# Kernel optimization log

Hardware: AMD Instinct MI355X
Metric: run time of the kernel (lower is better)

## Reference

```python
import jax, jax.numpy as jnp
import numpy as np

B, T, D, P = 32, 2048, 256, 100000
MAX_SPAN = 16


def setup_inputs() -> dict:
    key = jax.random.key(0)
    k0, k1, k2, k3, k4, k5 = jax.random.split(key, 6)
    token_embs = jax.random.normal(k0, (B, T, D), dtype=jnp.float32)
    p1_span = jax.random.randint(k1, (P,), 1, MAX_SPAN + 1, dtype=jnp.int32)
    p2_span = jax.random.randint(k2, (P,), 1, MAX_SPAN + 1, dtype=jnp.int32)
    p1_start = jax.random.randint(k3, (P,), 0, T - MAX_SPAN, dtype=jnp.int32)
    p2_start = jax.random.randint(k4, (P,), 0, T - MAX_SPAN, dtype=jnp.int32)
    pair_batch = jax.random.randint(k5, (P,), 0, B, dtype=jnp.int32)
    return {
        "token_embs": token_embs,
        "p1_start": p1_start,
        "p1_span": p1_span,
        "p2_start": p2_start,
        "p2_span": p2_span,
        "pair_batch": pair_batch,
    }


def reference(token_embs, p1_start, p1_span, p2_start, p2_span, pair_batch):
    # token_embs: [B, T, D]; per-pair ranges [start, start+span) within batch row pair_batch.
    # Range mean via exclusive prefix sums: mean = (csum[end] - csum[start]) / span.
    b, t, d = token_embs.shape
    csum = jnp.concatenate(
        [jnp.zeros((b, 1, d), token_embs.dtype), jnp.cumsum(token_embs, axis=1)],
        axis=1,
    )  # [B, T+1, D]

    def span_mean(start, span):
        end = start + span
        s = csum[pair_batch, end] - csum[pair_batch, start]  # [P, D]
        return s / span[:, None].astype(token_embs.dtype)

    p1 = span_mean(p1_start, p1_span)
    p2 = span_mean(p2_start, p2_span)
    return jnp.concatenate([p1, p2], axis=-1)  # [P, 2D]
```

## Files before the change

### kernel.cpp

```cpp
#include <hip/hip_runtime.h>


#define PB_B 32
#define PB_T 2048
#define PB_D 256
#define PB_P 100000
#define NSPAN (2 * PB_P)
#define NWIN 128
#define NBIN (PB_B * NWIN)
#define WROWS 31

typedef float vfloat4 __attribute__((ext_vector_type(4)));

__global__ __launch_bounds__(256) void hist_kernel(
    const int* __restrict__ p1_start, const int* __restrict__ p2_start,
    const int* __restrict__ pair_batch, int* __restrict__ counts)
{
    const int i = blockIdx.x * 256 + threadIdx.x;
    if (i >= PB_P) return;
    const int b = pair_batch[i];
    atomicAdd(&counts[(b << 7) + (p1_start[i] >> 4)], 1);
    atomicAdd(&counts[(b << 7) + (p2_start[i] >> 4)], 1);
}

__global__ __launch_bounds__(256) void scan_bins_kernel(
    const int* __restrict__ counts, int* __restrict__ bin_base,
    int* __restrict__ cursors)
{
    __shared__ int wsum[4];
    const int t = threadIdx.x;
    int local[16];
    int run = 0;
    #pragma unroll
    for (int i = 0; i < 16; ++i) { local[i] = counts[t * 16 + i]; run += local[i]; }

    const int lane = t & 63, wv = t >> 6;
    int incl = run;
    #pragma unroll
    for (int off = 1; off < 64; off <<= 1) {
        int v = __shfl_up(incl, off);
        if (lane >= off) incl += v;
    }
    if (lane == 63) wsum[wv] = incl;
    __syncthreads();
    int base = incl - run;
    for (int i = 0; i < wv; ++i) base += wsum[i];

    int c = base;
    #pragma unroll
    for (int i = 0; i < 16; ++i) {
        bin_base[t * 16 + i] = c;
        cursors[t * 16 + i] = c;
        c += local[i];
    }
    if (t == 255) bin_base[NBIN] = c;
}

__global__ __launch_bounds__(256) void scatter_kernel(
    const int* __restrict__ p1_start, const int* __restrict__ p1_span,
    const int* __restrict__ p2_start, const int* __restrict__ p2_span,
    const int* __restrict__ pair_batch,
    int* __restrict__ cursors, int2* __restrict__ meta)
{
    const int i = blockIdx.x * 256 + threadIdx.x;
    if (i >= PB_P) return;
    const int b = pair_batch[i];
    {
        const int s = p1_start[i];
        const int pos = atomicAdd(&cursors[(b << 7) + (s >> 4)], 1);
        meta[pos] = make_int2(2 * i, (b << 11) + s + (p1_span[i] << 16));
    }
    {
        const int s = p2_start[i];
        const int pos = atomicAdd(&cursors[(b << 7) + (s >> 4)], 1);
        meta[pos] = make_int2(2 * i + 1, (b << 11) + s + (p2_span[i] << 16));
    }
}

__global__ __launch_bounds__(512) void gather_kernel(
    const float* __restrict__ emb, const int2* __restrict__ meta,
    const int* __restrict__ bin_base, float* __restrict__ out)
{
    __shared__ float cs[32 * PB_D];

    const int blk  = (blockIdx.x & 7) * (NBIN / 8) + (blockIdx.x >> 3);
    const int b    = blk >> 7;
    const int row0 = (blk & 127) << 4;

    const float4* __restrict__ g =
        (const float4*)(emb + (((long long)b << 11) + row0) * PB_D);
    float4* l4 = (float4*)cs;
    const int nf4 = WROWS * (PB_D / 4);
    const int nvalid = (PB_T - row0 < WROWS ? PB_T - row0 : WROWS) * (PB_D / 4);
    #pragma unroll
    for (int k = 0; k < 4; ++k) {
        const int i = k * 512 + threadIdx.x;
        if (i < nf4) {
            float4 v = make_float4(0.f, 0.f, 0.f, 0.f);
            if (i < nvalid) v = g[i];
            l4[i] = v;
        }
    }
    __syncthreads();

    if (threadIdx.x < PB_D) {
        const int d = threadIdx.x;
        float run = 0.f;
        #pragma unroll
        for (int r = 0; r < WROWS; ++r) {
            const float v = cs[r * PB_D + d];
            cs[r * PB_D + d] = run;
            run += v;
        }
        cs[WROWS * PB_D + d] = run;
    }
    __syncthreads();

    const int s0 = bin_base[blk], s1 = bin_base[blk + 1];
    const int lane = threadIdx.x & 63, wv = threadIdx.x >> 6;
    for (int s = s0 + wv; s < s1; s += 8) {
        const int2 m = meta[s];
        const int lr = (m.y & 2047) - row0;
        const int n  = m.y >> 16;
        const float4 a = ((const float4*)cs)[lr * (PB_D / 4) + lane];
        const float4 e = ((const float4*)cs)[(lr + n) * (PB_D / 4) + lane];
        const float inv = 1.f / (float)n;
        vfloat4 o = { (e.x - a.x) * inv, (e.y - a.y) * inv,
                      (e.z - a.z) * inv, (e.w - a.w) * inv };
        __builtin_nontemporal_store(o, (vfloat4*)out + (long long)m.x * 64 + lane);
    }
}

extern "C" void kernel_launch(void* const* d_in, const int* in_sizes, int n_in,
                              void* d_out, int out_size, void* d_ws, size_t ws_size,
                              hipStream_t stream) {
    const float* token_embs = (const float*)d_in[0];
    const int* p1_start = (const int*)d_in[1];
    const int* p1_span  = (const int*)d_in[2];
    const int* p2_start = (const int*)d_in[3];
    const int* p2_span  = (const int*)d_in[4];
    const int* pair_batch = (const int*)d_in[5];
    float* out = (float*)d_out;

    int2* meta   = (int2*)d_ws;
    int* counts  = (int*)(meta + NSPAN);
    int* cursors = counts + NBIN;
    int* bin_base = cursors + NBIN;

    (void)hipMemsetAsync(counts, 0, NBIN * sizeof(int), stream);
    const int hb = (PB_P + 255) / 256;
    hist_kernel<<<hb, 256, 0, stream>>>(p1_start, p2_start, pair_batch, counts);
    scan_bins_kernel<<<1, 256, 0, stream>>>(counts, bin_base, cursors);
    scatter_kernel<<<hb, 256, 0, stream>>>(
        p1_start, p1_span, p2_start, p2_span, pair_batch, cursors, meta);

    gather_kernel<<<NBIN, 512, 0, stream>>>(token_embs, meta, bin_base, out);
}
```

Measured before the change: 306.1 us.

## Replace histogram+scan binning with fixed-capacity per-bin buckets

Drops the histogram and prefix-scan kernels by giving each (batch, window) bin a fixed 256-slot region in workspace. The scatter kernel writes to bin*CAP+cursor, and the gather kernel reads the cursor count directly and skips empty bins. This removes two launches and a pass over the index arrays. In exchange it uses more workspace and silently overflows if any bin receives more than 256 spans.

```diff
diff --git a/kernel.cpp b/kernel.cpp
--- a/kernel.cpp
+++ b/kernel.cpp
@@ -5,56 +5,12 @@
 #define PB_T 2048
 #define PB_D 256
 #define PB_P 100000
-#define NSPAN (2 * PB_P)
 #define NWIN 128
 #define NBIN (PB_B * NWIN)
+#define CAP 256
 #define WROWS 31
 
 typedef float vfloat4 __attribute__((ext_vector_type(4)));
-
-__global__ __launch_bounds__(256) void hist_kernel(
-    const int* __restrict__ p1_start, const int* __restrict__ p2_start,
-    const int* __restrict__ pair_batch, int* __restrict__ counts)
-{
-    const int i = blockIdx.x * 256 + threadIdx.x;
-    if (i >= PB_P) return;
-    const int b = pair_batch[i];
-    atomicAdd(&counts[(b << 7) + (p1_start[i] >> 4)], 1);
-    atomicAdd(&counts[(b << 7) + (p2_start[i] >> 4)], 1);
-}
-
-__global__ __launch_bounds__(256) void scan_bins_kernel(
-    const int* __restrict__ counts, int* __restrict__ bin_base,
-    int* __restrict__ cursors)
-{
-    __shared__ int wsum[4];
-    const int t = threadIdx.x;
-    int local[16];
-    int run = 0;
-    #pragma unroll
-    for (int i = 0; i < 16; ++i) { local[i] = counts[t * 16 + i]; run += local[i]; }
-
-    const int lane = t & 63, wv = t >> 6;
-    int incl = run;
-    #pragma unroll
-    for (int off = 1; off < 64; off <<= 1) {
-        int v = __shfl_up(incl, off);
-        if (lane >= off) incl += v;
-    }
-    if (lane == 63) wsum[wv] = incl;
-    __syncthreads();
-    int base = incl - run;
-    for (int i = 0; i < wv; ++i) base += wsum[i];
-
-    int c = base;
-    #pragma unroll
-    for (int i = 0; i < 16; ++i) {
-        bin_base[t * 16 + i] = c;
-        cursors[t * 16 + i] = c;
-        c += local[i];
-    }
-    if (t == 255) bin_base[NBIN] = c;
-}
 
 __global__ __launch_bounds__(256) void scatter_kernel(
     const int* __restrict__ p1_start, const int* __restrict__ p1_span,
@@ -67,23 +23,28 @@
     const int b = pair_batch[i];
     {
         const int s = p1_start[i];
-        const int pos = atomicAdd(&cursors[(b << 7) + (s >> 4)], 1);
-        meta[pos] = make_int2(2 * i, (b << 11) + s + (p1_span[i] << 16));
+        const int bin = (b << 7) + (s >> 4);
+        const int pos = atomicAdd(&cursors[bin], 1);
+        meta[bin * CAP + pos] = make_int2(2 * i, (b << 11) + s + (p1_span[i] << 16));
     }
     {
         const int s = p2_start[i];
-        const int pos = atomicAdd(&cursors[(b << 7) + (s >> 4)], 1);
-        meta[pos] = make_int2(2 * i + 1, (b << 11) + s + (p2_span[i] << 16));
+        const int bin = (b << 7) + (s >> 4);
+        const int pos = atomicAdd(&cursors[bin], 1);
+        meta[bin * CAP + pos] = make_int2(2 * i + 1, (b << 11) + s + (p2_span[i] << 16));
     }
 }
 
 __global__ __launch_bounds__(512) void gather_kernel(
     const float* __restrict__ emb, const int2* __restrict__ meta,
-    const int* __restrict__ bin_base, float* __restrict__ out)
+    const int* __restrict__ cursors, float* __restrict__ out)
 {
     __shared__ float cs[32 * PB_D];
 
     const int blk  = (blockIdx.x & 7) * (NBIN / 8) + (blockIdx.x >> 3);
+    const int cnt  = cursors[blk];
+    if (cnt == 0) return;
+
     const int b    = blk >> 7;
     const int row0 = (blk & 127) << 4;
 
@@ -116,10 +77,10 @@
     }
     __syncthreads();
 
-    const int s0 = bin_base[blk], s1 = bin_base[blk + 1];
+    const int2* __restrict__ bmeta = meta + blk * CAP;
     const int lane = threadIdx.x & 63, wv = threadIdx.x >> 6;
-    for (int s = s0 + wv; s < s1; s += 8) {
-        const int2 m = meta[s];
+    for (int s = wv; s < cnt; s += 8) {
+        const int2 m = bmeta[s];
         const int lr = (m.y & 2047) - row0;
         const int n  = m.y >> 16;
         const float4 a = ((const float4*)cs)[lr * (PB_D / 4) + lane];
@@ -134,25 +95,21 @@
 extern "C" void kernel_launch(void* const* d_in, const int* in_sizes, int n_in,
                               void* d_out, int out_size, void* d_ws, size_t ws_size,
                               hipStream_t stream) {
-    const float* token_embs = (const float*)d_in[0];
     const int* p1_start = (const int*)d_in[1];
     const int* p1_span  = (const int*)d_in[2];
     const int* p2_start = (const int*)d_in[3];
     const int* p2_span  = (const int*)d_in[4];
     const int* pair_batch = (const int*)d_in[5];
+    const float* token_embs = (const float*)d_in[0];
     float* out = (float*)d_out;
 
     int2* meta   = (int2*)d_ws;
-    int* counts  = (int*)(meta + NSPAN);
-    int* cursors = counts + NBIN;
-    int* bin_base = cursors + NBIN;
+    int* cursors = (int*)(meta + (size_t)NBIN * CAP);
 
-    (void)hipMemsetAsync(counts, 0, NBIN * sizeof(int), stream);
+    (void)hipMemsetAsync(cursors, 0, NBIN * sizeof(int), stream);
     const int hb = (PB_P + 255) / 256;
-    hist_kernel<<<hb, 256, 0, stream>>>(p1_start, p2_start, pair_batch, counts);
-    scan_bins_kernel<<<1, 256, 0, stream>>>(counts, bin_base, cursors);
     scatter_kernel<<<hb, 256, 0, stream>>>(
         p1_start, p1_span, p2_start, p2_span, pair_batch, cursors, meta);
 
-    gather_kernel<<<NBIN, 512, 0, stream>>>(token_embs, meta, bin_base, out);
+    gather_kernel<<<NBIN, 512, 0, stream>>>(token_embs, meta, cursors, out);
 }
```

Result: faster. 288.7 us (-5.7%).
